# Performance work log

Hardware: AMD Instinct MI355X
Metric: run time of the kernel (lower is better)

The kernel has to match this reference:

```python
import jax, jax.numpy as jnp
import numpy as np

B, D, C = 8192, 2048, 1000

def setup_inputs() -> dict:
    key = jax.random.key(0)
    k1, k2, k3 = jax.random.split(key, 3)
    x = jax.random.normal(k1, (B, D), dtype=jnp.float32)
    W = jax.random.normal(k2, (D, C), dtype=jnp.float32) * (1.0 / np.sqrt(D))
    b = jax.random.normal(k3, (C,), dtype=jnp.float32) * 0.01
    return {"x": x, "W": W, "b": b}

def reference(x, W, b):
    # inner classifier: logits out[b, c]
    out = jnp.dot(x, W) + b  # [B, C]
    # leave-one-out logsumexp per class, fused:
    # lse_k = logsumexp(out[:, != k]) = lse_all + log1p(-exp(out_k - lse_all))
    lse = jax.nn.logsumexp(out, axis=1, keepdims=True)  # [B, 1]
    loo = lse + jnp.log1p(-jnp.exp(out - lse))           # [B, C]
    # c_out = -loo; return c_out + out
    return out - loo
```

## Files before the change

kernel.cpp:

```cpp
#include <hip/hip_runtime.h>
#include <hip/hip_bf16.h>
#include <math.h>

#define BDIM 8192
#define DDIM 2048
#define CDIM 1000
#define NPAD 1024
#define BK   64

#define WS_BT_OFFSET  33554432ULL
#define WS_P0_OFFSET  37748736ULL
#define WS_P1_OFFSET  54132736ULL
#define WS_NEED       70516736ULL

typedef __attribute__((ext_vector_type(8))) short short8;
typedef __attribute__((ext_vector_type(4))) float floatx4;

__device__ __forceinline__ unsigned short f2bf(float f) {
    union { float f; unsigned u; } a; a.f = f;
    unsigned u = a.u;
    u = (u + 0x7fff + ((u >> 16) & 1)) >> 16;
    return (unsigned short)u;
}

__device__ __forceinline__ float bf2f(unsigned short h) {
    union { unsigned u; float f; } a; a.u = ((unsigned)h) << 16;
    return a.f;
}

__device__ __forceinline__ void async_copy16(const void* gp, void* lp) {
    __builtin_amdgcn_global_load_lds(
        (const __attribute__((address_space(1))) void*)gp,
        (__attribute__((address_space(3))) void*)lp,
        16, 0, 0);
}

__global__ __launch_bounds__(256) void cvt_kernel(
    const float* __restrict__ x, unsigned short* __restrict__ xb,
    const float* __restrict__ W, unsigned short* __restrict__ Bt)
{
    const int blk = blockIdx.x;
    const int t   = threadIdx.x;
    if (blk < 16384) {
        int i = blk * 256 + t;
        float4 v = ((const float4*)x)[i];
        ushort4 o;
        o.x = f2bf(v.x); o.y = f2bf(v.y); o.z = f2bf(v.z); o.w = f2bf(v.w);
        ((ushort4*)xb)[i] = o;
    } else {
        __shared__ float tile[32][33];
        const int b2 = blk - 16384;
        const int k0 = (b2 & 63) * 32;
        const int n0 = (b2 >> 6) * 32;
        const int tx = t & 31, ty = t >> 5;
        #pragma unroll
        for (int i = 0; i < 4; i++) {
            int k = k0 + ty + i * 8;
            int n = n0 + tx;
            tile[ty + i * 8][tx] = (n < CDIM) ? W[(size_t)k * CDIM + n] : 0.0f;
        }
        __syncthreads();
        #pragma unroll
        for (int i = 0; i < 4; i++) {
            int n = n0 + ty + i * 8;
            int k = k0 + tx;
            Bt[(size_t)n * DDIM + k] = f2bf(tile[tx][ty + i * 8]);
        }
    }
}

template <bool BF16OUT>
__device__ __forceinline__ void gemm_body(
    const unsigned short* __restrict__ A,
    const unsigned short* __restrict__ Bt,
    void* __restrict__ Cv,
    int mBase, int nBase, int kBase, int kIters,
    unsigned short* As, unsigned short* Bs)
{
    const int t    = threadIdx.x;
    const int wave = t >> 6;
    const int lane = t & 63;
    const int wm   = wave & 1;
    const int wn   = wave >> 1;
    const int quad = lane >> 4;
    const int l16  = lane & 15;

    floatx4 acc[4][4] = {};

    const int rowA = t >> 3;
    const int csw  = ((t & 7) ^ (rowA & 7)) * 16;
    const char* Ag = (const char*)A  + ((size_t)(mBase + rowA) * DDIM + kBase) * 2 + csw;
    const char* Bg = (const char*)Bt + ((size_t)(nBase + rowA) * DDIM + kBase) * 2 + csw;
    char* AsDst = (char*)As + t * 16;
    char* BsDst = (char*)Bs + t * 16;

    const int xorb0 = ((0 * 4 + quad) ^ (l16 & 7)) * 8;
    const int xorb1 = ((1 * 4 + quad) ^ (l16 & 7)) * 8;

    for (int kt = 0; kt < kIters * BK; kt += BK) {
        const char* a = Ag + kt * 2;
        const char* b = Bg + kt * 2;
        #pragma unroll
        for (int r = 0; r < 4; r++) {
            async_copy16(a + (size_t)r * 32 * DDIM * 2, AsDst + r * 4096);
            async_copy16(b + (size_t)r * 32 * DDIM * 2, BsDst + r * 4096);
        }
        __syncthreads();

        #pragma unroll
        for (int ks = 0; ks < 2; ks++) {
            const int xorb = ks ? xorb1 : xorb0;
            short8 af[4], bfr[4];
            #pragma unroll
            for (int mi = 0; mi < 4; mi++)
                af[mi] = *(const short8*)(As + (wm * 64 + mi * 16 + l16) * BK + xorb);
            #pragma unroll
            for (int ni = 0; ni < 4; ni++)
                bfr[ni] = *(const short8*)(Bs + (wn * 64 + ni * 16 + l16) * BK + xorb);
            #pragma unroll
            for (int mi = 0; mi < 4; mi++)
                #pragma unroll
                for (int ni = 0; ni < 4; ni++)
                    acc[mi][ni] = __builtin_amdgcn_mfma_f32_16x16x32_bf16(
                        af[mi], bfr[ni], acc[mi][ni], 0, 0, 0);
        }
        __syncthreads();
    }

    #pragma unroll
    for (int mi = 0; mi < 4; mi++) {
        int row0 = mBase + wm * 64 + mi * 16 + quad * 4;
        #pragma unroll
        for (int ni = 0; ni < 4; ni++) {
            int col = nBase + wn * 64 + ni * 16 + l16;
            if (col < CDIM) {
                #pragma unroll
                for (int rg = 0; rg < 4; rg++) {
                    if (BF16OUT)
                        ((unsigned short*)Cv)[(size_t)(row0 + rg) * CDIM + col] =
                            f2bf(acc[mi][ni][rg]);
                    else
                        ((float*)Cv)[(size_t)(row0 + rg) * CDIM + col] = acc[mi][ni][rg];
                }
            }
        }
    }
}

__global__ __launch_bounds__(256, 2) void gemm_single_kernel(
    const unsigned short* __restrict__ A,
    const unsigned short* __restrict__ Bt,
    float* __restrict__ C0)
{
    __shared__ unsigned short As[128 * BK];
    __shared__ unsigned short Bs[128 * BK];

    const int L   = blockIdx.x;
    const int xcd = L & 7;
    const int s   = L >> 3;
    const int m_t = xcd * 8 + (s >> 3);
    const int n_t = s & 7;

    gemm_body<false>(A, Bt, C0, m_t * 128, n_t * 128, 0, DDIM / BK, As, Bs);
}


#define STAGE_A(BUF, EXT, KO)                                                 \
    do {                                                                      \
        _Pragma("unroll")                                                     \
        for (int h = 0; h < 2; h++) {                                         \
            const int row_ = rA0 + (EXT) + h * 128;                           \
            async_copy16(gA + (size_t)row_ * DDIM + (KO),                     \
                         &As[BUF][row_ * BK + c8]);                           \
        }                                                                     \
    } while (0)

#define STAGE_B(BUF, EXT, KO)                                                 \
    do {                                                                      \
        _Pragma("unroll")                                                     \
        for (int h = 0; h < 2; h++) {                                         \
            const int row_ = rB0 + (EXT) + h * 128;                           \
            async_copy16(gB + (size_t)row_ * DDIM + (KO),                     \
                         &Bs[BUF][row_ * BK + c8]);                           \
        }                                                                     \
    } while (0)

#define LOADA(BUF, MQ)                                                        \
    do {                                                                      \
        _Pragma("unroll")                                                     \
        for (int mf = 0; mf < 4; mf++) {                                      \
            const int r_ = (arA + (MQ) * 64 + mf * 16) * BK;                  \
            af[mf][0] = *(const short8*)&As[BUF][r_ + xorb0];                 \
            af[mf][1] = *(const short8*)&As[BUF][r_ + xorb1];                 \
        }                                                                     \
    } while (0)

#define LOADB(BUF, NQ, BF)                                                    \
    do {                                                                      \
        _Pragma("unroll")                                                     \
        for (int nf = 0; nf < 2; nf++) {                                      \
            const int r_ = (arB + (NQ) * 32 + nf * 16) * BK;                  \
            BF[nf][0] = *(const short8*)&Bs[BUF][r_ + xorb0];                 \
            BF[nf][1] = *(const short8*)&Bs[BUF][r_ + xorb1];                 \
        }                                                                     \
    } while (0)

#define MMAC(MQ, NQ, BF)                                                      \
    do {                                                                      \
        __builtin_amdgcn_s_setprio(1);                                        \
        _Pragma("unroll")                                                     \
        for (int mf = 0; mf < 4; mf++) {                                      \
            _Pragma("unroll")                                                 \
            for (int nf = 0; nf < 2; nf++) {                                  \
                floatx4 c_ = acc[(MQ) * 4 + mf][(NQ) * 2 + nf];               \
                c_ = __builtin_amdgcn_mfma_f32_16x16x32_bf16(                 \
                    af[mf][0], BF[nf][0], c_, 0, 0, 0);                       \
                c_ = __builtin_amdgcn_mfma_f32_16x16x32_bf16(                 \
                    af[mf][1], BF[nf][1], c_, 0, 0, 0);                       \
                acc[(MQ) * 4 + mf][(NQ) * 2 + nf] = c_;                       \
            }                                                                 \
        }                                                                     \
        __builtin_amdgcn_s_setprio(0);                                        \
    } while (0)

#define RAW_BARRIER() asm volatile("s_barrier" ::: "memory")

__global__ __launch_bounds__(512) void gemm8_kernel(
    const unsigned short* __restrict__ A,
    const unsigned short* __restrict__ Bt,
    unsigned short* __restrict__ P0, unsigned short* __restrict__ P1)
{
    __shared__ unsigned short As[2][256 * BK];
    __shared__ unsigned short Bs[2][256 * BK];

    const int t    = threadIdx.x;
    const int wave = t >> 6;
    const int lane = t & 63;
    const int wm   = wave >> 2;
    const int wn   = wave & 3;
    const int quad = lane >> 4;
    const int l16  = lane & 15;

    const int L    = blockIdx.x;
    const int g    = (L & 7) * 32 + (L >> 3);
    const int z    = g & 1;
    const int tid2 = g >> 1;
    const int mBase = (tid2 >> 2) * 256;
    const int nBase = (tid2 & 3) * 256;
    const int kBase = z * (DDIM / 2);
    const int NTt   = (DDIM / 2) / BK;

    const int c8  = (t & 7) << 3;
    const int q0  = t >> 3;
    const int csw = (((t & 7) ^ (q0 & 7)) << 3);
    const int rA0 = q0;
    const int rB0 = q0 + (q0 & 32);
    const unsigned short* gA = A  + (size_t)mBase * DDIM + kBase + csw;
    const unsigned short* gB = Bt + (size_t)nBase * DDIM + kBase + csw;

    const int xorb0 = ((0 * 4 + quad) ^ (l16 & 7)) << 3;
    const int xorb1 = ((1 * 4 + quad) ^ (l16 & 7)) << 3;
    const int arA = wm * 128 + l16;
    const int arB = wn * 64 + l16;

    floatx4 acc[8][4] = {};
    short8 af[4][2], bf0[2][2], bf1[2][2];

    STAGE_A(0, 0, 0);
    STAGE_A(0, 64, 0);
    STAGE_B(0, 0, 0);
    STAGE_B(0, 32, 0);
    STAGE_A(1, 0, BK);
    STAGE_B(1, 0, BK);
    STAGE_B(1, 32, BK);
    asm volatile("s_waitcnt vmcnt(6)" ::: "memory");
    RAW_BARRIER();

    for (int j = 0; j < NTt; j++) {
        const int buf = j & 1;
        const int ko1 = (j + 1) * BK;
        const int ko2 = (j + 2) * BK;
        const bool s1 = (j + 1 < NTt);
        const bool s2 = (j + 2 < NTt);

        if (buf == 0) { LOADA(0, 0); LOADB(0, 0, bf0); }
        else          { LOADA(1, 0); LOADB(1, 0, bf0); }
        if (s1) { if (buf == 0) STAGE_A(1, 64, ko1); else STAGE_A(0, 64, ko1); }
        RAW_BARRIER();
        MMAC(0, 0, bf0);
        RAW_BARRIER();

        if (buf == 0) LOADB(0, 1, bf1); else LOADB(1, 1, bf1);
        if (s2) { if (buf == 0) STAGE_A(0, 0, ko2); else STAGE_A(1, 0, ko2); }
        RAW_BARRIER();
        MMAC(0, 1, bf1);
        RAW_BARRIER();

        if (buf == 0) LOADA(0, 1); else LOADA(1, 1);
        if (s2) { if (buf == 0) STAGE_B(0, 0, ko2); else STAGE_B(1, 0, ko2); }
        RAW_BARRIER();
        MMAC(1, 0, bf0);
        RAW_BARRIER();

        if (s2) { if (buf == 0) STAGE_B(0, 32, ko2); else STAGE_B(1, 32, ko2); }
        if (j < NTt - 3) asm volatile("s_waitcnt vmcnt(6)" ::: "memory");
        else             asm volatile("s_waitcnt vmcnt(0)" ::: "memory");
        RAW_BARRIER();
        MMAC(1, 1, bf1);
        RAW_BARRIER();
    }

    unsigned short* P = z ? P1 : P0;
    #pragma unroll
    for (int mfg = 0; mfg < 8; mfg++) {
        const int row0 = mBase + wm * 128 + mfg * 16 + quad * 4;
        #pragma unroll
        for (int nfg = 0; nfg < 4; nfg++) {
            const int col = nBase + wn * 64 + nfg * 16 + l16;
            if (col < CDIM) {
                #pragma unroll
                for (int rg = 0; rg < 4; rg++)
                    P[(size_t)(row0 + rg) * CDIM + col] = f2bf(acc[mfg][nfg][rg]);
            }
        }
    }
}

__global__ __launch_bounds__(256) void lse_kernel(
    float* __restrict__ out,
    const unsigned short* P0, const unsigned short* P1,
    const float* __restrict__ bias, int split)
{
    const int row = blockIdx.x;
    const int t   = threadIdx.x;
    __shared__ float red[8];

    const bool valid = t < (CDIM / 4);
    const int c0 = t * 4;

    float4 v = make_float4(-INFINITY, -INFINITY, -INFINITY, -INFINITY);
    float4 e = make_float4(0.f, 0.f, 0.f, 0.f);
    if (valid) {
        if (split) {
            ushort4 p0 = *(const ushort4*)(P0 + (size_t)row * CDIM + c0);
            ushort4 p1 = *(const ushort4*)(P1 + (size_t)row * CDIM + c0);
            v.x = bf2f(p0.x) + bf2f(p1.x);
            v.y = bf2f(p0.y) + bf2f(p1.y);
            v.z = bf2f(p0.z) + bf2f(p1.z);
            v.w = bf2f(p0.w) + bf2f(p1.w);
        } else {
            v = *(const float4*)(out + (size_t)row * CDIM + c0);
        }
        float4 bb = *(const float4*)(bias + c0);
        v.x += bb.x; v.y += bb.y; v.z += bb.z; v.w += bb.w;
    }

    float m = fmaxf(fmaxf(v.x, v.y), fmaxf(v.z, v.w));
    #pragma unroll
    for (int off = 32; off > 0; off >>= 1)
        m = fmaxf(m, __shfl_down(m, off, 64));
    const int wave = t >> 6;
    if ((t & 63) == 0) red[wave] = m;
    __syncthreads();
    if (t == 0) red[4] = fmaxf(fmaxf(red[0], red[1]), fmaxf(red[2], red[3]));
    __syncthreads();
    const float M = red[4];

    float s = 0.f;
    if (valid) {
        e.x = expf(v.x - M); e.y = expf(v.y - M);
        e.z = expf(v.z - M); e.w = expf(v.w - M);
        s = e.x + e.y + e.z + e.w;
    }
    #pragma unroll
    for (int off = 32; off > 0; off >>= 1)
        s += __shfl_down(s, off, 64);
    if ((t & 63) == 0) red[wave] = s;
    __syncthreads();
    if (t == 0) red[4] = red[0] + red[1] + red[2] + red[3];
    __syncthreads();
    const float S    = red[4];
    const float lse  = M + logf(S);
    const float invS = 1.0f / S;

    if (valid) {
        float4 o;
        o.x = (v.x - lse) - log1pf(-e.x * invS);
        o.y = (v.y - lse) - log1pf(-e.y * invS);
        o.z = (v.z - lse) - log1pf(-e.z * invS);
        o.w = (v.w - lse) - log1pf(-e.w * invS);
        *(float4*)(out + (size_t)row * CDIM + c0) = o;
    }
}

extern "C" void kernel_launch(void* const* d_in, const int* in_sizes, int n_in,
                              void* d_out, int out_size, void* d_ws, size_t ws_size,
                              hipStream_t stream) {
    const float* x = (const float*)d_in[0];
    const float* W = (const float*)d_in[1];
    const float* b = (const float*)d_in[2];
    float* out = (float*)d_out;

    unsigned short* xb = (unsigned short*)d_ws;
    unsigned short* Bt = (unsigned short*)((char*)d_ws + WS_BT_OFFSET);
    unsigned short* P0 = (unsigned short*)((char*)d_ws + WS_P0_OFFSET);
    unsigned short* P1 = (unsigned short*)((char*)d_ws + WS_P1_OFFSET);
    const bool splitk = ws_size >= WS_NEED;

    cvt_kernel<<<18432, 256, 0, stream>>>(x, xb, W, Bt);

    if (splitk) {
        gemm8_kernel<<<256, 512, 0, stream>>>(xb, Bt, P0, P1);
        lse_kernel<<<BDIM, 256, 0, stream>>>(out, P0, P1, b, 1);
    } else {
        gemm_single_kernel<<<512, 256, 0, stream>>>(xb, Bt, out);
        lse_kernel<<<BDIM, 256, 0, stream>>>(out, nullptr, nullptr, b, 0);
    }
}
```

Before: 178.1 us.

## Restructure GEMM main loop to overlap LDS fragment loads with MFMA phases

Rewrites the double-buffered bf16 GEMM loop so each phase issues the next LDS fragment loads right after the MFMA batch, halving barrier count per iteration (4 instead of 8). The next tile's first A/B fragments are prefetched at the end of each iteration, and the buffer selection uses pointer offsets instead of branch duplication. Global staging order and vmcnt thresholds are rebalanced. Risk: relies on MFMA/ds_read interleaving and correct waitcnt accounting; register pressure from overlapping fragments may rise.

Result: no change. 175.6 us (-1.4%).

```diff
diff --git a/kernel.cpp b/kernel.cpp
--- a/kernel.cpp
+++ b/kernel.cpp
@@ -165,43 +165,45 @@
 }
 
 
-#define STAGE_A(BUF, EXT, KO)                                                 \
+#define HBUF (256 * BK)
+
+#define STAGE_A2(BASE, EXT, KO)                                               \
     do {                                                                      \
         _Pragma("unroll")                                                     \
         for (int h = 0; h < 2; h++) {                                         \
             const int row_ = rA0 + (EXT) + h * 128;                           \
             async_copy16(gA + (size_t)row_ * DDIM + (KO),                     \
-                         &As[BUF][row_ * BK + c8]);                           \
+                         (BASE) + row_ * BK + c8);                            \
         }                                                                     \
     } while (0)
 
-#define STAGE_B(BUF, EXT, KO)                                                 \
+#define STAGE_B2(BASE, EXT, KO)                                               \
     do {                                                                      \
         _Pragma("unroll")                                                     \
         for (int h = 0; h < 2; h++) {                                         \
             const int row_ = rB0 + (EXT) + h * 128;                           \
             async_copy16(gB + (size_t)row_ * DDIM + (KO),                     \
-                         &Bs[BUF][row_ * BK + c8]);                           \
+                         (BASE) + row_ * BK + c8);                            \
         }                                                                     \
     } while (0)
 
-#define LOADA(BUF, MQ)                                                        \
+#define LOADA_(BASE, MQ)                                                      \
     do {                                                                      \
         _Pragma("unroll")                                                     \
         for (int mf = 0; mf < 4; mf++) {                                      \
             const int r_ = (arA + (MQ) * 64 + mf * 16) * BK;                  \
-            af[mf][0] = *(const short8*)&As[BUF][r_ + xorb0];                 \
-            af[mf][1] = *(const short8*)&As[BUF][r_ + xorb1];                 \
+            af[mf][0] = *(const short8*)((BASE) + r_ + xorb0);                \
+            af[mf][1] = *(const short8*)((BASE) + r_ + xorb1);                \
         }                                                                     \
     } while (0)
 
-#define LOADB(BUF, NQ, BF)                                                    \
+#define LOADB_(BASE, NQ, BF)                                                  \
     do {                                                                      \
         _Pragma("unroll")                                                     \
         for (int nf = 0; nf < 2; nf++) {                                      \
             const int r_ = (arB + (NQ) * 32 + nf * 16) * BK;                  \
-            BF[nf][0] = *(const short8*)&Bs[BUF][r_ + xorb0];                 \
-            BF[nf][1] = *(const short8*)&Bs[BUF][r_ + xorb1];                 \
+            BF[nf][0] = *(const short8*)((BASE) + r_ + xorb0);                \
+            BF[nf][1] = *(const short8*)((BASE) + r_ + xorb1);                \
         }                                                                     \
     } while (0)
 
@@ -224,14 +226,16 @@
     } while (0)
 
 #define RAW_BARRIER() asm volatile("s_barrier" ::: "memory")
+#define WAIT_VM(N)    asm volatile("s_waitcnt vmcnt(" #N ")" ::: "memory")
+#define WAIT_LGKM0()  asm volatile("s_waitcnt lgkmcnt(0)" ::: "memory")
 
 __global__ __launch_bounds__(512) void gemm8_kernel(
     const unsigned short* __restrict__ A,
     const unsigned short* __restrict__ Bt,
     unsigned short* __restrict__ P0, unsigned short* __restrict__ P1)
 {
-    __shared__ unsigned short As[2][256 * BK];
-    __shared__ unsigned short Bs[2][256 * BK];
+    __shared__ unsigned short As[2 * HBUF];
+    __shared__ unsigned short Bs[2 * HBUF];
 
     const int t    = threadIdx.x;
     const int wave = t >> 6;
@@ -266,47 +270,50 @@
     floatx4 acc[8][4] = {};
     short8 af[4][2], bf0[2][2], bf1[2][2];
 
-    STAGE_A(0, 0, 0);
-    STAGE_A(0, 64, 0);
-    STAGE_B(0, 0, 0);
-    STAGE_B(0, 32, 0);
-    STAGE_A(1, 0, BK);
-    STAGE_B(1, 0, BK);
-    STAGE_B(1, 32, BK);
-    asm volatile("s_waitcnt vmcnt(6)" ::: "memory");
+    STAGE_A2(As, 0, 0);
+    STAGE_A2(As, 64, 0);
+    STAGE_B2(Bs, 0, 0);
+    STAGE_B2(Bs, 32, 0);
+    STAGE_A2(As + HBUF, 0, BK);
+    STAGE_A2(As + HBUF, 64, BK);
+    STAGE_B2(Bs + HBUF, 0, BK);
+    STAGE_B2(Bs + HBUF, 32, BK);
+    WAIT_VM(8);
     RAW_BARRIER();
+    LOADA_(As, 0);
+    LOADB_(Bs, 0, bf0);
+    WAIT_LGKM0();
+    RAW_BARRIER();
 
     for (int j = 0; j < NTt; j++) {
-        const int buf = j & 1;
-        const int ko1 = (j + 1) * BK;
-        const int ko2 = (j + 2) * BK;
-        const bool s1 = (j + 1 < NTt);
-        const bool s2 = (j + 2 < NTt);
-
-        if (buf == 0) { LOADA(0, 0); LOADB(0, 0, bf0); }
-        else          { LOADA(1, 0); LOADB(1, 0, bf0); }
-        if (s1) { if (buf == 0) STAGE_A(1, 64, ko1); else STAGE_A(0, 64, ko1); }
+        const int bo = (j & 1) * HBUF;
+        unsigned short* const cA = (unsigned short*)As + bo;
+        unsigned short* const cB = (unsigned short*)Bs + bo;
+        const unsigned short* const nA = (const unsigned short*)As + (bo ^ HBUF);
+        const unsigned short* const nB = (const unsigned short*)Bs + (bo ^ HBUF);
+        const int  ko2 = (j + 2) * BK;
+        const bool s2  = (j + 2 < NTt);
+
+        if (s2) STAGE_A2(cA, 0, ko2);
+        MMAC(0, 0, bf0);
+        LOADB_(cB, 1, bf1);
         RAW_BARRIER();
-        MMAC(0, 0, bf0);
+
+        if (s2) STAGE_B2(cB, 0, ko2);
+        MMAC(0, 1, bf1);
+        LOADA_(cA, 1);
         RAW_BARRIER();
 
-        if (buf == 0) LOADB(0, 1, bf1); else LOADB(1, 1, bf1);
-        if (s2) { if (buf == 0) STAGE_A(0, 0, ko2); else STAGE_A(1, 0, ko2); }
+        if (s2) STAGE_B2(cB, 32, ko2);
+        MMAC(1, 0, bf0);
+        if (j < NTt - 2) WAIT_VM(6);
+        else             WAIT_VM(0);
         RAW_BARRIER();
-        MMAC(0, 1, bf1);
-        RAW_BARRIER();
-
-        if (buf == 0) LOADA(0, 1); else LOADA(1, 1);
-        if (s2) { if (buf == 0) STAGE_B(0, 0, ko2); else STAGE_B(1, 0, ko2); }
-        RAW_BARRIER();
-        MMAC(1, 0, bf0);
-        RAW_BARRIER();
-
-        if (s2) { if (buf == 0) STAGE_B(0, 32, ko2); else STAGE_B(1, 32, ko2); }
-        if (j < NTt - 3) asm volatile("s_waitcnt vmcnt(6)" ::: "memory");
-        else             asm volatile("s_waitcnt vmcnt(0)" ::: "memory");
-        RAW_BARRIER();
+
+        if (s2) STAGE_A2(cA, 64, ko2);
         MMAC(1, 1, bf1);
+        if (j + 1 < NTt) { LOADA_(nA, 0); LOADB_(nB, 0, bf0); }
+        WAIT_LGKM0();
         RAW_BARRIER();
     }
 
```
